# Optimization experiments

Hardware: AMD Instinct MI355X
Metric: run time of the kernel (lower is better)

## Reference

```python
import jax, jax.numpy as jnp
import numpy as np

NUM_SITES_X = 2048
NUM_SITES_Y = 4096
NUM_CLB_SITES = 6_000_000
NUM_SLICE_SITES = 6_000_000
NUM_SITES = NUM_SITES_X * NUM_SITES_Y  # global flattened site-id space


def setup_inputs() -> dict:
    key = jax.random.key(0)
    k1, k2, k3, k4 = jax.random.split(key, 4)
    # CLB slice site ids (x*num_sites_y + y), sorted as produced from the column-major fabric scan
    slice_sites = jnp.sort(
        jax.random.randint(k1, (NUM_SLICE_SITES,), 0, NUM_SITES, dtype=jnp.int32))
    # per-CLB-site signature count; >0 means the site already has instances committed
    site_det_sig_idx = jax.random.randint(
        k2, (NUM_CLB_SITES,), 0, 4, dtype=jnp.int32)
    # compact CLB address -> global site id map (monotone by construction in the original)
    addr2site_map = jnp.sort(
        jax.random.randint(k3, (NUM_CLB_SITES,), 0, NUM_SITES, dtype=jnp.int32))
    # per-slice-site legalization score (site_det_score analogue)
    site_scores = jax.random.normal(k4, (NUM_SLICE_SITES,), dtype=jnp.float32)
    return {
        "slice_sites": slice_sites,
        "site_det_sig_idx": site_det_sig_idx,
        "addr2site_map": addr2site_map,
        "site_scores": site_scores,
    }


def _remaining_mask(slice_sites, site_det_sig_idx, addr2site_map):
    """Faithful jit-friendly version of compute_remaining_slice_sites.

    torch/np original:
      assigned = addr2site_map[site_det_sig_idx > 0]
      mask[np.in1d(slice_sites, assigned)] = True; return ~mask
    We avoid the data-dependent boolean gather by replacing unassigned
    entries with a -1 sentinel (site ids are >= 0), sorting, and doing a
    vectorized membership test via searchsorted.
    """
    n = addr2site_map.shape[0]
    assigned = jnp.where(site_det_sig_idx > 0, addr2site_map, jnp.int32(-1))
    assigned_sorted = jnp.sort(assigned)  # sentinels land at the front
    pos = jnp.searchsorted(assigned_sorted, slice_sites, side="left")
    pos = jnp.clip(pos, 0, n - 1)
    found = assigned_sorted[pos] == slice_sites  # in1d membership
    return ~found  # True where the slice site is still available


def reference(slice_sites, site_det_sig_idx, addr2site_map, site_scores):
    remaining = _remaining_mask(slice_sites, site_det_sig_idx, addr2site_map)
    # scores of still-available candidate sites (zeros where already assigned)
    avail_scores = jnp.where(remaining, site_scores, jnp.zeros((), site_scores.dtype))
    return remaining, avail_scores
```

## Files before the change

kernel.cpp:

```cpp
#include <hip/hip_runtime.h>


typedef int   v4i __attribute__((ext_vector_type(4)));
typedef float v4f __attribute__((ext_vector_type(4)));

static constexpr int NUM_SITES_TOTAL = 2048 * 4096;
static constexpr int BITMAP_WORDS    = NUM_SITES_TOTAL / 32;
static constexpr int WORDS_PER_BLOCK = 128;
static constexpr int SITES_PER_BLOCK = WORDS_PER_BLOCK * 32;
static constexpr int MARK_BLOCKS     = BITMAP_WORDS / WORDS_PER_BLOCK;
static constexpr int BLOCK           = 256;
static constexpr int CHUNK           = 16;

__global__ __launch_bounds__(BLOCK) void mark_kernel(
    const int* __restrict__ sig, const int* __restrict__ a2s,
    unsigned int* __restrict__ bm, int n_clb)
{
    __shared__ unsigned int lbm[WORDS_PER_BLOCK];

    const int siteBase = blockIdx.x * SITES_PER_BLOCK;
    const int siteEnd  = siteBase + SITES_PER_BLOCK;

    for (int w = threadIdx.x; w < WORDS_PER_BLOCK; w += BLOCK) lbm[w] = 0u;

    int lo = 0, hi = n_clb;
    while (lo < hi) { int m = (lo + hi) >> 1; if (a2s[m] < siteBase) lo = m + 1; else hi = m; }
    const int e0 = lo;
    hi = n_clb;
    while (lo < hi) { int m = (lo + hi) >> 1; if (a2s[m] < siteEnd) lo = m + 1; else hi = m; }
    const int e1 = lo;

    __syncthreads();

    const int start = e0 & ~(CHUNK - 1);

    for (int s = start + threadIdx.x * CHUNK; s < e1; s += BLOCK * CHUNK) {
        int av[CHUNK], gv[CHUNK];
        if (s + CHUNK <= n_clb) {
            const v4i* ap = (const v4i*)(a2s + s);
            const v4i* gp = (const v4i*)(sig + s);
#pragma unroll
            for (int q = 0; q < CHUNK / 4; ++q) {
                v4i a = ap[q];
                av[4*q+0] = a.x; av[4*q+1] = a.y; av[4*q+2] = a.z; av[4*q+3] = a.w;
                v4i g = gp[q];
                gv[4*q+0] = g.x; gv[4*q+1] = g.y; gv[4*q+2] = g.z; gv[4*q+3] = g.w;
            }
        } else {
#pragma unroll
            for (int j = 0; j < CHUNK; ++j) {
                const int i = s + j;
                const bool ok = i < n_clb;
                av[j] = ok ? a2s[i] : -1;
                gv[j] = ok ? sig[i] : 0;
            }
        }

        unsigned int curw = 0xFFFFFFFFu, curm = 0u;
#pragma unroll
        for (int j = 0; j < CHUNK; ++j) {
            const int site = av[j];
            if (gv[j] > 0 && site >= siteBase && site < siteEnd) {
                const unsigned int u = (unsigned int)(site - siteBase);
                const unsigned int w = u >> 5;
                const unsigned int m = 1u << (u & 31u);
                if (w == curw) {
                    curm |= m;
                } else {
                    if (curm) atomicOr(&lbm[curw], curm);
                    curw = w; curm = m;
                }
            }
        }
        if (curm) atomicOr(&lbm[curw], curm);
    }

    __syncthreads();

    uint4* dst = (uint4*)(bm + blockIdx.x * WORDS_PER_BLOCK);
    const uint4* src = (const uint4*)lbm;
    for (int q = threadIdx.x; q < WORDS_PER_BLOCK / 4; q += BLOCK) dst[q] = src[q];
}

__global__ __launch_bounds__(BLOCK) void probe_kernel(
    const int* __restrict__ ss, const float* __restrict__ sc,
    const unsigned int* __restrict__ bm,
    float* __restrict__ rem, float* __restrict__ avail, int n8)
{
    const int t = blockIdx.x * BLOCK + threadIdx.x;
    if (t >= n8) return;
    const int base = t * 8;

    const v4i* sp = (const v4i*)(ss + base);
    const v4f* cp = (const v4f*)(sc + base);
    v4i s01 = __builtin_nontemporal_load(sp);
    v4i s23 = __builtin_nontemporal_load(sp + 1);
    v4f f01 = __builtin_nontemporal_load(cp);
    v4f f23 = __builtin_nontemporal_load(cp + 1);

    int   sv[8] = {s01.x, s01.y, s01.z, s01.w, s23.x, s23.y, s23.z, s23.w};
    float fv[8] = {f01.x, f01.y, f01.z, f01.w, f23.x, f23.y, f23.z, f23.w};
    float rv[8], av[8];
#pragma unroll
    for (int j = 0; j < 8; ++j) {
        const unsigned int u = (unsigned int)sv[j];
        const unsigned int bit = (bm[u >> 5] >> (u & 31u)) & 1u;
        rv[j] = bit ? 0.0f : 1.0f;
        av[j] = bit ? 0.0f : fv[j];
    }

    v4f* rp = (v4f*)(rem + base);
    v4f* ap = (v4f*)(avail + base);
    v4f r0 = {rv[0], rv[1], rv[2], rv[3]};
    v4f r1 = {rv[4], rv[5], rv[6], rv[7]};
    v4f a0 = {av[0], av[1], av[2], av[3]};
    v4f a1 = {av[4], av[5], av[6], av[7]};
    __builtin_nontemporal_store(r0, rp);
    __builtin_nontemporal_store(r1, rp + 1);
    __builtin_nontemporal_store(a0, ap);
    __builtin_nontemporal_store(a1, ap + 1);
}

__global__ void probe_tail_kernel(
    const int* __restrict__ ss, const float* __restrict__ sc,
    const unsigned int* __restrict__ bm,
    float* __restrict__ rem, float* __restrict__ avail, int start, int n)
{
    const int i = start + blockIdx.x * blockDim.x + threadIdx.x;
    if (i >= n) return;
    const unsigned int u = (unsigned int)ss[i];
    const unsigned int bit = (bm[u >> 5] >> (u & 31u)) & 1u;
    rem[i]   = bit ? 0.0f : 1.0f;
    avail[i] = bit ? 0.0f : sc[i];
}

extern "C" void kernel_launch(void* const* d_in, const int* in_sizes, int n_in,
                              void* d_out, int out_size, void* d_ws, size_t ws_size,
                              hipStream_t stream) {
    const int*   slice_sites = (const int*)d_in[0];
    const int*   sig         = (const int*)d_in[1];
    const int*   a2s         = (const int*)d_in[2];
    const float* scores      = (const float*)d_in[3];
    const int n_slice = in_sizes[0];
    const int n_clb   = in_sizes[1];

    unsigned int* bm = (unsigned int*)d_ws;

    mark_kernel<<<MARK_BLOCKS, BLOCK, 0, stream>>>(sig, a2s, bm, n_clb);

    float* rem   = (float*)d_out;
    float* avail = rem + n_slice;
    const int n8 = n_slice / 8;
    if (n8 > 0)
        probe_kernel<<<(n8 + BLOCK - 1) / BLOCK, BLOCK, 0, stream>>>(
            slice_sites, scores, bm, rem, avail, n8);
    if (n8 * 8 < n_slice)
        probe_tail_kernel<<<1, 64, 0, stream>>>(slice_sites, scores, bm,
                                                rem, avail, n8 * 8, n_slice);
}
```

Measured before the change: 151.5 us.

## Fuse bitmap marking and probe into one kernel using sorted slice sites

Merges the mark and probe kernels into one kernel. Each block builds its shared-memory bitmap for its range of site ids, then binary-searches the sorted slice_sites array for the same range and probes the local bitmap directly. This removes the global bitmap write and read, the random gathers into it, and two extra launches. In exchange it relies on slice_sites being sorted, adds two more binary searches per block, and has uneven per-block work with only 2048 blocks.

```diff
diff --git a/kernel.cpp b/kernel.cpp
--- a/kernel.cpp
+++ b/kernel.cpp
@@ -5,16 +5,20 @@
 typedef float v4f __attribute__((ext_vector_type(4)));
 
 static constexpr int NUM_SITES_TOTAL = 2048 * 4096;
-static constexpr int BITMAP_WORDS    = NUM_SITES_TOTAL / 32;
 static constexpr int WORDS_PER_BLOCK = 128;
 static constexpr int SITES_PER_BLOCK = WORDS_PER_BLOCK * 32;
-static constexpr int MARK_BLOCKS     = BITMAP_WORDS / WORDS_PER_BLOCK;
+static constexpr int GRID            = NUM_SITES_TOTAL / SITES_PER_BLOCK;
 static constexpr int BLOCK           = 256;
 static constexpr int CHUNK           = 16;
 
-__global__ __launch_bounds__(BLOCK) void mark_kernel(
-    const int* __restrict__ sig, const int* __restrict__ a2s,
-    unsigned int* __restrict__ bm, int n_clb)
+__global__ __launch_bounds__(BLOCK) void fused_kernel(
+    const int*   __restrict__ ss,
+    const int*   __restrict__ sig,
+    const int*   __restrict__ a2s,
+    const float* __restrict__ sc,
+    float*       __restrict__ rem,
+    float*       __restrict__ avail,
+    int n_slice, int n_clb)
 {
     __shared__ unsigned int lbm[WORDS_PER_BLOCK];
 
@@ -30,10 +34,16 @@
     while (lo < hi) { int m = (lo + hi) >> 1; if (a2s[m] < siteEnd) lo = m + 1; else hi = m; }
     const int e1 = lo;
 
+    lo = 0; hi = n_slice;
+    while (lo < hi) { int m = (lo + hi) >> 1; if (ss[m] < siteBase) lo = m + 1; else hi = m; }
+    const int p0 = lo;
+    hi = n_slice;
+    while (lo < hi) { int m = (lo + hi) >> 1; if (ss[m] < siteEnd) lo = m + 1; else hi = m; }
+    const int p1 = lo;
+
     __syncthreads();
 
     const int start = e0 & ~(CHUNK - 1);
-
     for (int s = start + threadIdx.x * CHUNK; s < e1; s += BLOCK * CHUNK) {
         int av[CHUNK], gv[CHUNK];
         if (s + CHUNK <= n_clb) {
@@ -64,12 +74,8 @@
                 const unsigned int u = (unsigned int)(site - siteBase);
                 const unsigned int w = u >> 5;
                 const unsigned int m = 1u << (u & 31u);
-                if (w == curw) {
-                    curm |= m;
-                } else {
-                    if (curm) atomicOr(&lbm[curw], curm);
-                    curw = w; curm = m;
-                }
+                if (w == curw) curm |= m;
+                else { if (curm) atomicOr(&lbm[curw], curm); curw = w; curm = m; }
             }
         }
         if (curm) atomicOr(&lbm[curw], curm);
@@ -77,61 +83,36 @@
 
     __syncthreads();
 
-    uint4* dst = (uint4*)(bm + blockIdx.x * WORDS_PER_BLOCK);
-    const uint4* src = (const uint4*)lbm;
-    for (int q = threadIdx.x; q < WORDS_PER_BLOCK / 4; q += BLOCK) dst[q] = src[q];
-}
+    int i0 = (p0 + 3) & ~3;
+    int i1 = p1 & ~3;
+    if (i1 < i0) i1 = i0;
 
-__global__ __launch_bounds__(BLOCK) void probe_kernel(
-    const int* __restrict__ ss, const float* __restrict__ sc,
-    const unsigned int* __restrict__ bm,
-    float* __restrict__ rem, float* __restrict__ avail, int n8)
-{
-    const int t = blockIdx.x * BLOCK + threadIdx.x;
-    if (t >= n8) return;
-    const int base = t * 8;
-
-    const v4i* sp = (const v4i*)(ss + base);
-    const v4f* cp = (const v4f*)(sc + base);
-    v4i s01 = __builtin_nontemporal_load(sp);
-    v4i s23 = __builtin_nontemporal_load(sp + 1);
-    v4f f01 = __builtin_nontemporal_load(cp);
-    v4f f23 = __builtin_nontemporal_load(cp + 1);
-
-    int   sv[8] = {s01.x, s01.y, s01.z, s01.w, s23.x, s23.y, s23.z, s23.w};
-    float fv[8] = {f01.x, f01.y, f01.z, f01.w, f23.x, f23.y, f23.z, f23.w};
-    float rv[8], av[8];
+    for (int q = (i0 >> 2) + threadIdx.x; q < (i1 >> 2); q += BLOCK) {
+        v4i s = __builtin_nontemporal_load((const v4i*)ss + q);
+        v4f f = __builtin_nontemporal_load((const v4f*)sc + q);
+        v4f r, a;
 #pragma unroll
-    for (int j = 0; j < 8; ++j) {
-        const unsigned int u = (unsigned int)sv[j];
-        const unsigned int bit = (bm[u >> 5] >> (u & 31u)) & 1u;
-        rv[j] = bit ? 0.0f : 1.0f;
-        av[j] = bit ? 0.0f : fv[j];
+        for (int j = 0; j < 4; ++j) {
+            const unsigned int u   = (unsigned int)(s[j] - siteBase);
+            const unsigned int bit = (lbm[u >> 5] >> (u & 31u)) & 1u;
+            r[j] = bit ? 0.0f : 1.0f;
+            a[j] = bit ? 0.0f : f[j];
+        }
+        __builtin_nontemporal_store(r, (v4f*)rem + q);
+        __builtin_nontemporal_store(a, (v4f*)avail + q);
     }
-
-    v4f* rp = (v4f*)(rem + base);
-    v4f* ap = (v4f*)(avail + base);
-    v4f r0 = {rv[0], rv[1], rv[2], rv[3]};
-    v4f r1 = {rv[4], rv[5], rv[6], rv[7]};
-    v4f a0 = {av[0], av[1], av[2], av[3]};
-    v4f a1 = {av[4], av[5], av[6], av[7]};
-    __builtin_nontemporal_store(r0, rp);
-    __builtin_nontemporal_store(r1, rp + 1);
-    __builtin_nontemporal_store(a0, ap);
-    __builtin_nontemporal_store(a1, ap + 1);
-}
-
-__global__ void probe_tail_kernel(
-    const int* __restrict__ ss, const float* __restrict__ sc,
-    const unsigned int* __restrict__ bm,
-    float* __restrict__ rem, float* __restrict__ avail, int start, int n)
-{
-    const int i = start + blockIdx.x * blockDim.x + threadIdx.x;
-    if (i >= n) return;
-    const unsigned int u = (unsigned int)ss[i];
-    const unsigned int bit = (bm[u >> 5] >> (u & 31u)) & 1u;
-    rem[i]   = bit ? 0.0f : 1.0f;
-    avail[i] = bit ? 0.0f : sc[i];
+    for (int i = p0 + threadIdx.x; i < min(i0, p1); i += BLOCK) {
+        const unsigned int u   = (unsigned int)(ss[i] - siteBase);
+        const unsigned int bit = (lbm[u >> 5] >> (u & 31u)) & 1u;
+        rem[i]   = bit ? 0.0f : 1.0f;
+        avail[i] = bit ? 0.0f : sc[i];
+    }
+    for (int i = max(i1, p0) + threadIdx.x; i < p1; i += BLOCK) {
+        const unsigned int u   = (unsigned int)(ss[i] - siteBase);
+        const unsigned int bit = (lbm[u >> 5] >> (u & 31u)) & 1u;
+        rem[i]   = bit ? 0.0f : 1.0f;
+        avail[i] = bit ? 0.0f : sc[i];
+    }
 }
 
 extern "C" void kernel_launch(void* const* d_in, const int* in_sizes, int n_in,
@@ -144,17 +125,9 @@
     const int n_slice = in_sizes[0];
     const int n_clb   = in_sizes[1];
 
-    unsigned int* bm = (unsigned int*)d_ws;
-
-    mark_kernel<<<MARK_BLOCKS, BLOCK, 0, stream>>>(sig, a2s, bm, n_clb);
-
     float* rem   = (float*)d_out;
     float* avail = rem + n_slice;
-    const int n8 = n_slice / 8;
-    if (n8 > 0)
-        probe_kernel<<<(n8 + BLOCK - 1) / BLOCK, BLOCK, 0, stream>>>(
-            slice_sites, scores, bm, rem, avail, n8);
-    if (n8 * 8 < n_slice)
-        probe_tail_kernel<<<1, 64, 0, stream>>>(slice_sites, scores, bm,
-                                                rem, avail, n8 * 8, n_slice);
+
+    fused_kernel<<<GRID, BLOCK, 0, stream>>>(
+        slice_sites, sig, a2s, scores, rem, avail, n_slice, n_clb);
 }
```

New measurement: 160.4 us. 1.06x slower.

## Partition bitmap marking by input tiles instead of per-block site ranges

Applied to the files above, without the earlier changes.

The mark kernel now gives each block a fixed tile of the sorted address map and builds a shared-memory window covering the site range that tile spans. This replaces the old per-output-block binary searches and redundant scans. Interior window words are written directly and the two edge words are merged with global atomicOr. Sites beyond the window fall back to global atomics. A separate zero kernel clears the bitmap first, which adds one launch and a full-bitmap write pass.

```diff
diff --git a/kernel.cpp b/kernel.cpp
--- a/kernel.cpp
+++ b/kernel.cpp
@@ -4,82 +4,83 @@
 typedef int   v4i __attribute__((ext_vector_type(4)));
 typedef float v4f __attribute__((ext_vector_type(4)));
 
-static constexpr int NUM_SITES_TOTAL = 2048 * 4096;
-static constexpr int BITMAP_WORDS    = NUM_SITES_TOTAL / 32;
-static constexpr int WORDS_PER_BLOCK = 128;
-static constexpr int SITES_PER_BLOCK = WORDS_PER_BLOCK * 32;
-static constexpr int MARK_BLOCKS     = BITMAP_WORDS / WORDS_PER_BLOCK;
-static constexpr int BLOCK           = 256;
-static constexpr int CHUNK           = 16;
+static constexpr int BITMAP_WORDS = (2048 * 4096) / 32;
+static constexpr int BLOCK        = 256;
+static constexpr int EPT          = 8;
+static constexpr int TILE         = BLOCK * EPT;
+static constexpr int WINDOW       = 4096;
+
+__global__ __launch_bounds__(BLOCK) void zero_kernel(uint4* __restrict__ bm) {
+    bm[blockIdx.x * BLOCK + threadIdx.x] = make_uint4(0u, 0u, 0u, 0u);
+}
 
 __global__ __launch_bounds__(BLOCK) void mark_kernel(
     const int* __restrict__ sig, const int* __restrict__ a2s,
-    unsigned int* __restrict__ bm, int n_clb)
+    unsigned int* __restrict__ bm, int n)
 {
-    __shared__ unsigned int lbm[WORDS_PER_BLOCK];
+    __shared__ unsigned int win[WINDOW];
+    __shared__ int s_lo, s_hi;
 
-    const int siteBase = blockIdx.x * SITES_PER_BLOCK;
-    const int siteEnd  = siteBase + SITES_PER_BLOCK;
+    const int blockStart = blockIdx.x * TILE;
+    const int e_end      = min(blockStart + TILE, n);
+    const int base       = blockStart + threadIdx.x * EPT;
+    const int cnt        = max(0, min(EPT, e_end - base));
 
-    for (int w = threadIdx.x; w < WORDS_PER_BLOCK; w += BLOCK) lbm[w] = 0u;
+    int av[EPT], gv[EPT];
+    if (cnt == EPT) {
+        v4i a0 = __builtin_nontemporal_load((const v4i*)(a2s + base));
+        v4i a1 = __builtin_nontemporal_load((const v4i*)(a2s + base + 4));
+        v4i g0 = __builtin_nontemporal_load((const v4i*)(sig + base));
+        v4i g1 = __builtin_nontemporal_load((const v4i*)(sig + base + 4));
+        av[0]=a0.x; av[1]=a0.y; av[2]=a0.z; av[3]=a0.w;
+        av[4]=a1.x; av[5]=a1.y; av[6]=a1.z; av[7]=a1.w;
+        gv[0]=g0.x; gv[1]=g0.y; gv[2]=g0.z; gv[3]=g0.w;
+        gv[4]=g1.x; gv[5]=g1.y; gv[6]=g1.z; gv[7]=g1.w;
+    } else {
+#pragma unroll
+        for (int j = 0; j < EPT; ++j) {
+            const int i = base + j;
+            const bool ok = i < e_end;
+            av[j] = ok ? a2s[i] : 0;
+            gv[j] = ok ? sig[i] : 0;
+        }
+    }
 
-    int lo = 0, hi = n_clb;
-    while (lo < hi) { int m = (lo + hi) >> 1; if (a2s[m] < siteBase) lo = m + 1; else hi = m; }
-    const int e0 = lo;
-    hi = n_clb;
-    while (lo < hi) { int m = (lo + hi) >> 1; if (a2s[m] < siteEnd) lo = m + 1; else hi = m; }
-    const int e1 = lo;
-
+    if (base == blockStart)            s_lo = av[0];
+    if (cnt > 0 && base + cnt == e_end) s_hi = av[cnt - 1];
     __syncthreads();
 
-    const int start = e0 & ~(CHUNK - 1);
+    const int winBase  = s_lo >> 5;
+    const int winWords = (s_hi >> 5) - winBase + 1;
+    const int wlim     = min(winWords, WINDOW);
 
-    for (int s = start + threadIdx.x * CHUNK; s < e1; s += BLOCK * CHUNK) {
-        int av[CHUNK], gv[CHUNK];
-        if (s + CHUNK <= n_clb) {
-            const v4i* ap = (const v4i*)(a2s + s);
-            const v4i* gp = (const v4i*)(sig + s);
+    for (int w = threadIdx.x; w < wlim; w += BLOCK) win[w] = 0u;
+    __syncthreads();
+
+    int curw = -1; unsigned int curm = 0u;
 #pragma unroll
-            for (int q = 0; q < CHUNK / 4; ++q) {
-                v4i a = ap[q];
-                av[4*q+0] = a.x; av[4*q+1] = a.y; av[4*q+2] = a.z; av[4*q+3] = a.w;
-                v4i g = gp[q];
-                gv[4*q+0] = g.x; gv[4*q+1] = g.y; gv[4*q+2] = g.z; gv[4*q+3] = g.w;
-            }
-        } else {
-#pragma unroll
-            for (int j = 0; j < CHUNK; ++j) {
-                const int i = s + j;
-                const bool ok = i < n_clb;
-                av[j] = ok ? a2s[i] : -1;
-                gv[j] = ok ? sig[i] : 0;
+    for (int j = 0; j < EPT; ++j) {
+        if (gv[j] > 0) {
+            const unsigned int site = (unsigned int)av[j];
+            const int w = (int)(site >> 5) - winBase;
+            const unsigned int m = 1u << (site & 31u);
+            if (w < WINDOW) {
+                if (w == curw) curm |= m;
+                else { if (curw >= 0) atomicOr(&win[curw], curm); curw = w; curm = m; }
+            } else {
+                atomicOr(bm + (site >> 5), m);
             }
         }
-
-        unsigned int curw = 0xFFFFFFFFu, curm = 0u;
-#pragma unroll
-        for (int j = 0; j < CHUNK; ++j) {
-            const int site = av[j];
-            if (gv[j] > 0 && site >= siteBase && site < siteEnd) {
-                const unsigned int u = (unsigned int)(site - siteBase);
-                const unsigned int w = u >> 5;
-                const unsigned int m = 1u << (u & 31u);
-                if (w == curw) {
-                    curm |= m;
-                } else {
-                    if (curm) atomicOr(&lbm[curw], curm);
-                    curw = w; curm = m;
-                }
-            }
-        }
-        if (curm) atomicOr(&lbm[curw], curm);
     }
-
+    if (curw >= 0) atomicOr(&win[curw], curm);
     __syncthreads();
 
-    uint4* dst = (uint4*)(bm + blockIdx.x * WORDS_PER_BLOCK);
-    const uint4* src = (const uint4*)lbm;
-    for (int q = threadIdx.x; q < WORDS_PER_BLOCK / 4; q += BLOCK) dst[q] = src[q];
+    for (int w = threadIdx.x; w < wlim; w += BLOCK) {
+        const unsigned int v = win[w];
+        const int g = winBase + w;
+        if (w == 0 || w == winWords - 1) { if (v) atomicOr(bm + g, v); }
+        else bm[g] = v;
+    }
 }
 
 __global__ __launch_bounds__(BLOCK) void probe_kernel(
@@ -91,34 +92,30 @@
     if (t >= n8) return;
     const int base = t * 8;
 
-    const v4i* sp = (const v4i*)(ss + base);
-    const v4f* cp = (const v4f*)(sc + base);
-    v4i s01 = __builtin_nontemporal_load(sp);
-    v4i s23 = __builtin_nontemporal_load(sp + 1);
-    v4f f01 = __builtin_nontemporal_load(cp);
-    v4f f23 = __builtin_nontemporal_load(cp + 1);
+    v4i s0 = __builtin_nontemporal_load((const v4i*)(ss + base));
+    v4i s1 = __builtin_nontemporal_load((const v4i*)(ss + base + 4));
+    v4f f0 = __builtin_nontemporal_load((const v4f*)(sc + base));
+    v4f f1 = __builtin_nontemporal_load((const v4f*)(sc + base + 4));
 
-    int   sv[8] = {s01.x, s01.y, s01.z, s01.w, s23.x, s23.y, s23.z, s23.w};
-    float fv[8] = {f01.x, f01.y, f01.z, f01.w, f23.x, f23.y, f23.z, f23.w};
+    int   sv[8] = {s0.x, s0.y, s0.z, s0.w, s1.x, s1.y, s1.z, s1.w};
+    float fv[8] = {f0.x, f0.y, f0.z, f0.w, f1.x, f1.y, f1.z, f1.w};
     float rv[8], av[8];
 #pragma unroll
     for (int j = 0; j < 8; ++j) {
-        const unsigned int u = (unsigned int)sv[j];
+        const unsigned int u   = (unsigned int)sv[j];
         const unsigned int bit = (bm[u >> 5] >> (u & 31u)) & 1u;
         rv[j] = bit ? 0.0f : 1.0f;
         av[j] = bit ? 0.0f : fv[j];
     }
 
-    v4f* rp = (v4f*)(rem + base);
-    v4f* ap = (v4f*)(avail + base);
     v4f r0 = {rv[0], rv[1], rv[2], rv[3]};
     v4f r1 = {rv[4], rv[5], rv[6], rv[7]};
     v4f a0 = {av[0], av[1], av[2], av[3]};
     v4f a1 = {av[4], av[5], av[6], av[7]};
-    __builtin_nontemporal_store(r0, rp);
-    __builtin_nontemporal_store(r1, rp + 1);
-    __builtin_nontemporal_store(a0, ap);
-    __builtin_nontemporal_store(a1, ap + 1);
+    __builtin_nontemporal_store(r0, (v4f*)(rem + base));
+    __builtin_nontemporal_store(r1, (v4f*)(rem + base + 4));
+    __builtin_nontemporal_store(a0, (v4f*)(avail + base));
+    __builtin_nontemporal_store(a1, (v4f*)(avail + base + 4));
 }
 
 __global__ void probe_tail_kernel(
@@ -128,7 +125,7 @@
 {
     const int i = start + blockIdx.x * blockDim.x + threadIdx.x;
     if (i >= n) return;
-    const unsigned int u = (unsigned int)ss[i];
+    const unsigned int u   = (unsigned int)ss[i];
     const unsigned int bit = (bm[u >> 5] >> (u & 31u)) & 1u;
     rem[i]   = bit ? 0.0f : 1.0f;
     avail[i] = bit ? 0.0f : sc[i];
@@ -137,24 +134,26 @@
 extern "C" void kernel_launch(void* const* d_in, const int* in_sizes, int n_in,
                               void* d_out, int out_size, void* d_ws, size_t ws_size,
                               hipStream_t stream) {
-    const int*   slice_sites = (const int*)d_in[0];
-    const int*   sig         = (const int*)d_in[1];
-    const int*   a2s         = (const int*)d_in[2];
-    const float* scores      = (const float*)d_in[3];
+    const int*   ss  = (const int*)d_in[0];
+    const int*   sig = (const int*)d_in[1];
+    const int*   a2s = (const int*)d_in[2];
+    const float* sc  = (const float*)d_in[3];
     const int n_slice = in_sizes[0];
     const int n_clb   = in_sizes[1];
 
     unsigned int* bm = (unsigned int*)d_ws;
 
-    mark_kernel<<<MARK_BLOCKS, BLOCK, 0, stream>>>(sig, a2s, bm, n_clb);
+    zero_kernel<<<BITMAP_WORDS / 4 / BLOCK, BLOCK, 0, stream>>>((uint4*)bm);
+
+    mark_kernel<<<(n_clb + TILE - 1) / TILE, BLOCK, 0, stream>>>(sig, a2s, bm, n_clb);
 
     float* rem   = (float*)d_out;
     float* avail = rem + n_slice;
     const int n8 = n_slice / 8;
     if (n8 > 0)
         probe_kernel<<<(n8 + BLOCK - 1) / BLOCK, BLOCK, 0, stream>>>(
-            slice_sites, scores, bm, rem, avail, n8);
+            ss, sc, bm, rem, avail, n8);
     if (n8 * 8 < n_slice)
-        probe_tail_kernel<<<1, 64, 0, stream>>>(slice_sites, scores, bm,
-                                                rem, avail, n8 * 8, n_slice);
+        probe_tail_kernel<<<1, 64, 0, stream>>>(ss, sc, bm, rem, avail,
+                                                n8 * 8, n_slice);
 }
```

New measurement: 146.4 us. -3.4%, faster.
